# Kernel tuning notes

Hardware: AMD Instinct MI355X
Metric: run time of the kernel (lower is better)

Reference implementation:

```python
import jax, jax.numpy as jnp
import numpy as np

H = 512; W = 512; C = 32; E = 32; NH = 2; HD = 16; B = 4; N = 50000
SHIFTS = jnp.array([[0, 0], [-1, 0], [1, 0], [0, 1], [-1, 1], [1, 1], [0, -1], [-1, -1], [1, -1]], dtype=jnp.int32)


def setup_inputs() -> dict:
    key = jax.random.key(0)
    ks = jax.random.split(key, 12)

    def coords(k):
        # unique BEV cells per sample -> well-defined coord->index lookup
        flat = jax.random.permutation(k, H * W)[:N]
        return jnp.stack([flat // W, flat % W], axis=-1).astype(jnp.int32)

    li_coors = jnp.stack([coords(jax.random.fold_in(ks[0], b)) for b in range(B)])
    ra_coors = jnp.stack([coords(jax.random.fold_in(ks[1], b)) for b in range(B)])
    li_feats = jax.random.normal(ks[2], (B, N, C), jnp.float32)
    ra_feats = jax.random.normal(ks[3], (B, N, C), jnp.float32)
    s = 0.1
    return {
        "li_feats": li_feats, "li_coors": li_coors,
        "ra_feats": ra_feats, "ra_coors": ra_coors,
        "w_qkv1": jax.random.normal(ks[4], (3 * E, E), jnp.float32) * s,
        "b_qkv1": jax.random.normal(ks[5], (3 * E,), jnp.float32) * s,
        "w_out1": jax.random.normal(ks[6], (E, E), jnp.float32) * s,
        "b_out1": jax.random.normal(ks[7], (E,), jnp.float32) * s,
        "w_qkv2": jax.random.normal(ks[8], (3 * E, E), jnp.float32) * s,
        "b_qkv2": jax.random.normal(ks[9], (3 * E,), jnp.float32) * s,
        "w_out2": jax.random.normal(ks[10], (E, E), jnp.float32) * s,
        "b_out2": jax.random.normal(ks[11], (E,), jnp.float32) * s,
    }


def _mha(q, kv, w_qkv, b_qkv, w_out, b_out):
    # q: [N,1,E], kv: [N,9,E]; torch MultiheadAttention (eval, dropout off)
    wq, wk, wv = jnp.split(w_qkv, 3, axis=0)
    bq, bk, bv = jnp.split(b_qkv, 3)
    n = q.shape[0]
    Q = (q @ wq.T + bq).reshape(n, 1, NH, HD)
    K = (kv @ wk.T + bk).reshape(n, 9, NH, HD)
    V = (kv @ wv.T + bv).reshape(n, 9, NH, HD)
    s = jnp.einsum('nqhd,nkhd->nhqk', Q, K) / jnp.sqrt(jnp.float32(HD))
    a = jax.nn.softmax(s, axis=-1)
    o = jnp.einsum('nhqk,nkhd->nqhd', a, V).reshape(n, E)
    return o @ w_out.T + b_out


def _gather_keys(q_coor, kv_coor, kv_feat):
    # dense grid lookup: BEV cell -> voxel index in kv (-1 if empty)
    nk = kv_coor.shape[0]
    grid = jnp.full((H * W,), -1, jnp.int32).at[kv_coor[:, 0] * W + kv_coor[:, 1]].set(
        jnp.arange(nk, dtype=jnp.int32))
    sh = q_coor[:, None, :] + SHIFTS[None]  # [N,9,2]
    valid = (sh[..., 0] >= 0) & (sh[..., 0] < H) & (sh[..., 1] >= 0) & (sh[..., 1] < W)
    flat = jnp.clip(sh[..., 0], 0, H - 1) * W + jnp.clip(sh[..., 1], 0, W - 1)
    idx = jnp.where(valid, grid[flat], -1)  # [N,9]
    keys = jnp.where((idx >= 0)[..., None], kv_feat[jnp.clip(idx, 0)], 0.0)
    return keys  # [N,9,C]


def _scatter(feat, coor):
    # PointPillarsScatter: place [N,C] voxel feats into dense [C,H,W] canvas
    flat = coor[:, 0] * W + coor[:, 1]
    return jnp.zeros((C, H * W), feat.dtype).at[:, flat].set(feat.T).reshape(C, H, W)


def _branch(q_feat, q_coor, kv_feat, kv_coor, w_qkv, b_qkv, w_out, b_out):
    keys = _gather_keys(q_coor, kv_coor, kv_feat)
    out = _mha(q_feat[:, None, :], keys, w_qkv, b_qkv, w_out, b_out)
    return _scatter(q_feat + out, q_coor)


def reference(li_feats, li_coors, ra_feats, ra_coors,
              w_qkv1, b_qkv1, w_out1, b_out1,
              w_qkv2, b_qkv2, w_out2, b_out2):
    vb = jax.vmap(_branch, in_axes=(0, 0, 0, 0, None, None, None, None))
    li_img = vb(li_feats, li_coors, ra_feats, ra_coors, w_qkv1, b_qkv1, w_out1, b_out1)
    ra_img = vb(ra_feats, ra_coors, li_feats, li_coors, w_qkv2, b_qkv2, w_out2, b_out2)
    return (li_img, ra_img)  # each [B, C, H, W]
```

## Files before the change

### kernel.cpp

```cpp
#include <hip/hip_runtime.h>

#define HH 512
#define WW 512
#define HWC (HH * WW)
#define NV 50000
#define NB 4
#define NR (NB * NV)
#define NQ (2 * NR)
#define KVROWS (NR + 1)

typedef unsigned int uint32;

static __device__ __forceinline__ float4 ld4(const float* p) {
    return *reinterpret_cast<const float4*>(p);
}
static __device__ __forceinline__ uint32 bf16rne(float x) {
    uint32 u = __float_as_uint(x);
    return (u + 0x7FFFu + ((u >> 16) & 1u)) >> 16;
}

static __device__ __forceinline__ float red16(float x) {
    float t;
    t = __int_as_float(__builtin_amdgcn_update_dpp(0, __float_as_int(x), 0xB1, 0xF, 0xF, true));
    x += t;
    t = __int_as_float(__builtin_amdgcn_update_dpp(0, __float_as_int(x), 0x4E, 0xF, 0xF, true));
    x += t;
    t = __int_as_float(__builtin_amdgcn_update_dpp(0, __float_as_int(x), 0x141, 0xF, 0xF, true));
    x += t;
    t = __int_as_float(__builtin_amdgcn_update_dpp(0, __float_as_int(x), 0x140, 0xF, 0xF, true));
    x += t;
    return x;
}

__global__ void k_fill(int4* __restrict__ p) {
    const int total = 2 * NB * HWC / 4;
    const int stride = gridDim.x * blockDim.x;
    const int4 v = make_int4(-1, -1, -1, -1);
    for (int i = blockIdx.x * blockDim.x + threadIdx.x; i < total; i += stride)
        p[i] = v;
}

__global__ void k_grid(const int* __restrict__ li_coors, const int* __restrict__ ra_coors,
                       int* __restrict__ grids) {
    int t = blockIdx.x * blockDim.x + threadIdx.x;
    if (t >= NQ) return;
    int set = t / NR;
    int r2 = t - set * NR;
    int b = r2 / NV;
    int n = r2 - b * NV;
    const int* co = (set == 0 ? li_coors : ra_coors) + (size_t)(b * NV + n) * 2;
    grids[(set * NB + b) * HWC + co[0] * WW + co[1]] = n;
}

__launch_bounds__(256)
__global__ void k_proj_kv(const float* __restrict__ li_feats, const float* __restrict__ ra_feats,
                          const float* __restrict__ w_qkv1, const float* __restrict__ b_qkv1,
                          const float* __restrict__ w_qkv2, const float* __restrict__ b_qkv2,
                          uint32* __restrict__ KV) {
    const int f = blockIdx.y;
    const float* feats = f ? ra_feats : li_feats;
    const float* wkv_g = f ? w_qkv1 : w_qkv2;
    const float* bkv_g = f ? b_qkv1 : b_qkv2;

    __shared__ float xs[4][2][64];
    const int wave = threadIdx.x >> 6;
    const int l    = threadIdx.x & 63;
    const int h    = l >> 5;
    const int j    = l & 31;

    const int gw = blockIdx.x * 4 + wave;
    const int gs = gridDim.x * 4;

    int r0 = gw * 2;
    float xreg = feats[(size_t)r0 * 32 + l];

    float4 wk[8], wv[8];
#pragma unroll
    for (int i = 0; i < 8; ++i) {
        wk[i] = ld4(wkv_g + (32 + j) * 32 + i * 4);
        wv[i] = ld4(wkv_g + (64 + j) * 32 + i * 4);
    }
    const float bk = bkv_g[32 + j], bv = bkv_g[64 + j];

    uint32* KVb = KV + (size_t)(f ^ 1) * KVROWS * 32;

    if (blockIdx.x == 0 && threadIdx.x < 32)
        KVb[(size_t)NR * 32 + threadIdx.x] = bf16rne(bk) | (bf16rne(bv) << 16);

    int cur = 0;
    while (r0 < NR) {
        xs[wave][cur][l] = xreg;
        const int rn = r0 + gs * 2;
        if (rn < NR) xreg = feats[(size_t)rn * 32 + l];

        const float* xp = &xs[wave][cur][h * 32];
        float ak = bk, av = bv;
#pragma unroll
        for (int i = 0; i < 8; ++i) {
            float4 x = *reinterpret_cast<const float4*>(xp + i * 4);
            ak += x.x * wk[i].x + x.y * wk[i].y + x.z * wk[i].z + x.w * wk[i].w;
            av += x.x * wv[i].x + x.y * wv[i].y + x.z * wv[i].z + x.w * wv[i].w;
        }
        KVb[(size_t)(r0 + h) * 32 + j] = bf16rne(ak) | (bf16rne(av) << 16);
        r0 = rn;
        cur ^= 1;
    }
}

__global__ void k_nbr(const int* __restrict__ li_coors, const int* __restrict__ ra_coors,
                      const int* __restrict__ grids, int* __restrict__ nbr) {
    int q = blockIdx.x * 256 + threadIdx.x;
    if (q >= NQ) return;
    int br  = (q >= NR) ? 1 : 0;
    int rem = q - br * NR;
    int b   = rem / NV;
    const int* qc = br ? ra_coors : li_coors;
    const int* kvgrid = grids + ((br ^ 1) * NB + b) * HWC;
    const int2 rc = *reinterpret_cast<const int2*>(qc + (size_t)rem * 2);

    const int drs[9] = {0, -1, 1, 0, -1, 1, 0, -1, 1};
    const int dcs[9] = {0, 0, 0, 1, 1, 1, -1, -1, -1};
    const int base = b * NV;
    int v[9];
#pragma unroll
    for (int k = 0; k < 9; ++k) {
        int rr = rc.x + drs[k], cc = rc.y + dcs[k];
        bool valid = ((unsigned)rr < HH) & ((unsigned)cc < WW);
        int raw = kvgrid[valid ? rr * WW + cc : 0];
        int id = valid ? raw : -1;
        v[k] = (id >= 0 ? base + id : NR) * 128;
    }
    int4* np = reinterpret_cast<int4*>(nbr + (size_t)q * 12);
    np[0] = make_int4(v[0], v[1], v[2], v[3]);
    np[1] = make_int4(v[4], v[5], v[6], v[7]);
    np[2] = make_int4(v[8], 0, 0, 0);
}

__launch_bounds__(256)
__global__ void k_attn(const int* __restrict__ nbr,
                       const float* __restrict__ li_feats, const float* __restrict__ ra_feats,
                       const float* __restrict__ w_qkv1, const float* __restrict__ b_qkv1,
                       const float* __restrict__ w_out1, const float* __restrict__ b_out1,
                       const float* __restrict__ w_qkv2, const float* __restrict__ b_qkv2,
                       const float* __restrict__ w_out2, const float* __restrict__ b_out2,
                       const uint32* __restrict__ KV, float* __restrict__ res) {
    __shared__ float xs[8][4][32];
    __shared__ float os[8][4][32];
    const int g = threadIdx.x >> 5;
    const int j = threadIdx.x & 31;
    const int q0 = (blockIdx.x * 8 + g) * 4;
    const int br  = (q0 >= NR) ? 1 : 0;
    const int rem = q0 - br * NR;
    const float* feats = br ? ra_feats : li_feats;
    const float* wqkv  = br ? w_qkv2 : w_qkv1;
    const float* bqkv  = br ? b_qkv2 : b_qkv1;
    const float* wout  = br ? w_out2 : w_out1;
    const float* bout  = br ? b_out2 : b_out1;
    const char* KVbr = (const char*)(KV + (size_t)br * KVROWS * 32);

    int4 a0[4], a1[4], a2[4];
#pragma unroll
    for (int u = 0; u < 4; ++u) {
        const int4* np = reinterpret_cast<const int4*>(nbr + (size_t)(q0 + u) * 12);
        a0[u] = np[0]; a1[u] = np[1]; a2[u] = np[2];
    }

    float fr[4];
#pragma unroll
    for (int u = 0; u < 4; ++u) {
        fr[u] = feats[(size_t)(rem + u) * 32 + j];
        xs[g][u][j] = fr[u];
    }

    const int joff = j * 4;
    uint32 kvw[4][9];
#pragma unroll
    for (int u = 0; u < 4; ++u) {
        int off[9] = {a0[u].x, a0[u].y, a0[u].z, a0[u].w,
                      a1[u].x, a1[u].y, a1[u].z, a1[u].w, a2[u].x};
#pragma unroll
        for (int k = 0; k < 9; ++k)
            kvw[u][k] = *reinterpret_cast<const uint32*>(KVbr + (size_t)(unsigned)(off[k] + joff));
    }

    const float bq = bqkv[j];
    float Qf[4] = {bq, bq, bq, bq};
#pragma unroll
    for (int i = 0; i < 8; ++i) {
        float4 w = ld4(wqkv + j * 32 + i * 4);
#pragma unroll
        for (int u = 0; u < 4; ++u) {
            float4 x = *reinterpret_cast<const float4*>(&xs[g][u][i * 4]);
            Qf[u] += x.x * w.x + x.y * w.y + x.z * w.z + x.w * w.w;
        }
    }
    const float SC = 0.25f * 1.44269504f;
#pragma unroll
    for (int u = 0; u < 4; ++u) Qf[u] *= SC;

#pragma unroll
    for (int u = 0; u < 4; ++u) {
        float sum = 0.f, o = 0.f;
#pragma unroll
        for (int k = 0; k < 9; ++k) {
            float kk = __uint_as_float(kvw[u][k] << 16);
            float e = exp2f(red16(Qf[u] * kk));
            float vv = __uint_as_float(kvw[u][k] & 0xFFFF0000u);
            sum += e;
            o += e * vv;
        }
        os[g][u][j] = o / sum;
    }

    const float bo = bout[j];
    float outv[4] = {bo, bo, bo, bo};
#pragma unroll
    for (int i = 0; i < 8; ++i) {
        float4 w = ld4(wout + j * 32 + i * 4);
#pragma unroll
        for (int u = 0; u < 4; ++u) {
            float4 x = *reinterpret_cast<const float4*>(&os[g][u][i * 4]);
            outv[u] += x.x * w.x + x.y * w.y + x.z * w.z + x.w * w.w;
        }
    }
#pragma unroll
    for (int u = 0; u < 4; ++u)
        res[(size_t)(q0 + u) * 32 + j] = fr[u] + outv[u];
}

__launch_bounds__(256)
__global__ void k_densify(const int* __restrict__ grids, const float* __restrict__ res,
                          float* __restrict__ out) {
    int t = blockIdx.x * 256 + threadIdx.x;
    int plane = t >> 18;
    int s = t & (HWC - 1);
    int gidx = grids[t];
    float4 v[8];
    if (gidx >= 0) {
        const float* rp = res + ((size_t)plane * NV + gidx) * 32;
#pragma unroll
        for (int i = 0; i < 8; ++i) v[i] = ld4(rp + i * 4);
    } else {
#pragma unroll
        for (int i = 0; i < 8; ++i) v[i] = make_float4(0.f, 0.f, 0.f, 0.f);
    }
    float* ob = out + (size_t)plane * 32 * HWC + s;
#pragma unroll
    for (int i = 0; i < 8; ++i) {
        __builtin_nontemporal_store(v[i].x, ob + (size_t)(4 * i + 0) * HWC);
        __builtin_nontemporal_store(v[i].y, ob + (size_t)(4 * i + 1) * HWC);
        __builtin_nontemporal_store(v[i].z, ob + (size_t)(4 * i + 2) * HWC);
        __builtin_nontemporal_store(v[i].w, ob + (size_t)(4 * i + 3) * HWC);
    }
}

extern "C" void kernel_launch(void* const* d_in, const int* in_sizes, int n_in,
                              void* d_out, int out_size, void* d_ws, size_t ws_size,
                              hipStream_t stream) {
    const float* li_feats = (const float*)d_in[0];
    const int*   li_coors = (const int*)d_in[1];
    const float* ra_feats = (const float*)d_in[2];
    const int*   ra_coors = (const int*)d_in[3];
    const float* w_qkv1 = (const float*)d_in[4];
    const float* b_qkv1 = (const float*)d_in[5];
    const float* w_out1 = (const float*)d_in[6];
    const float* b_out1 = (const float*)d_in[7];
    const float* w_qkv2 = (const float*)d_in[8];
    const float* b_qkv2 = (const float*)d_in[9];
    const float* w_out2 = (const float*)d_in[10];
    const float* b_out2 = (const float*)d_in[11];
    float* out = (float*)d_out;

    char* ws = (char*)d_ws;
    size_t off = 0;
    int*    grids = (int*)(ws + off);    off += (size_t)2 * NB * HWC * 4;
    uint32* KV    = (uint32*)(ws + off); off += (size_t)2 * KVROWS * 32 * 4;
    float*  res   = (float*)(ws + off);  off += (size_t)NQ * 32 * 4;
    int*    nbr   = (int*)(ws + off);    off += (size_t)NQ * 12 * 4;

    k_fill<<<2048, 256, 0, stream>>>((int4*)grids);

    k_grid<<<(NQ + 255) / 256, 256, 0, stream>>>(li_coors, ra_coors, grids);

    k_proj_kv<<<dim3(3200, 2), 256, 0, stream>>>(
        li_feats, ra_feats, w_qkv1, b_qkv1, w_qkv2, b_qkv2, KV);

    k_nbr<<<(NQ + 255) / 256, 256, 0, stream>>>(li_coors, ra_coors, grids, nbr);

    k_attn<<<NQ / 32, 256, 0, stream>>>(
        nbr, li_feats, ra_feats,
        w_qkv1, b_qkv1, w_out1, b_out1,
        w_qkv2, b_qkv2, w_out2, b_out2,
        KV, res);

    k_densify<<<(2 * NB * HWC) / 256, 256, 0, stream>>>(grids, res, out);
}
```

Measured before the change: 272.2 us.

## Remap attention lanes so each handles 4 channels of one query with 16B KV loads

```diff
diff --git a/kernel.cpp b/kernel.cpp
--- a/kernel.cpp
+++ b/kernel.cpp
@@ -18,18 +18,10 @@
     uint32 u = __float_as_uint(x);
     return (u + 0x7FFFu + ((u >> 16) & 1u)) >> 16;
 }
-
-static __device__ __forceinline__ float red16(float x) {
-    float t;
-    t = __int_as_float(__builtin_amdgcn_update_dpp(0, __float_as_int(x), 0xB1, 0xF, 0xF, true));
-    x += t;
-    t = __int_as_float(__builtin_amdgcn_update_dpp(0, __float_as_int(x), 0x4E, 0xF, 0xF, true));
-    x += t;
-    t = __int_as_float(__builtin_amdgcn_update_dpp(0, __float_as_int(x), 0x141, 0xF, 0xF, true));
-    x += t;
-    t = __int_as_float(__builtin_amdgcn_update_dpp(0, __float_as_int(x), 0x140, 0xF, 0xF, true));
-    x += t;
-    return x;
+template <int CTRL>
+static __device__ __forceinline__ float dpp_add(float x) {
+    float t = __int_as_float(__builtin_amdgcn_update_dpp(0, __float_as_int(x), CTRL, 0xF, 0xF, true));
+    return x + t;
 }
 
 __global__ void k_fill(int4* __restrict__ p) {
@@ -145,12 +137,15 @@
                        const float* __restrict__ w_out2, const float* __restrict__ b_out2,
                        const uint32* __restrict__ KV, float* __restrict__ res) {
     __shared__ float xs[8][4][32];
-    __shared__ float os[8][4][32];
-    const int g = threadIdx.x >> 5;
-    const int j = threadIdx.x & 31;
-    const int q0 = (blockIdx.x * 8 + g) * 4;
-    const int br  = (q0 >= NR) ? 1 : 0;
-    const int rem = q0 - br * NR;
+    __shared__ float Qls[4][8][36];
+    __shared__ float os[4][8][36];
+    const int tid = threadIdx.x;
+    const int w = tid >> 6;
+    const int l = tid & 63;
+    const int g = tid >> 5;
+    const int j = tid & 31;
+    const int wq0 = (blockIdx.x * 4 + w) * 8;
+    const int br  = (wq0 >= NR) ? 1 : 0;
     const float* feats = br ? ra_feats : li_feats;
     const float* wqkv  = br ? w_qkv2 : w_qkv1;
     const float* bqkv  = br ? b_qkv2 : b_qkv1;
@@ -158,74 +153,76 @@
     const float* bout  = br ? b_out2 : b_out1;
     const char* KVbr = (const char*)(KV + (size_t)br * KVROWS * 32);
 
-    int4 a0[4], a1[4], a2[4];
+    const int qB = wq0 + (l >> 3);
+    const int4* np = reinterpret_cast<const int4*>(nbr + (size_t)qB * 12);
+    int4 b0 = np[0], b1 = np[1], b2 = np[2];
+    const int coff = (l & 7) * 16;
+    int off[9] = {b0.x, b0.y, b0.z, b0.w, b1.x, b1.y, b1.z, b1.w, b2.x};
+    uint4 kv4[9];
+#pragma unroll
+    for (int k = 0; k < 9; ++k)
+        kv4[k] = *reinterpret_cast<const uint4*>(KVbr + (size_t)(unsigned)(off[k] + coff));
+
+    const int qrow = (l >> 5) << 2;
+    const int remA = wq0 + qrow - br * NR;
+    float fr[4];
 #pragma unroll
     for (int u = 0; u < 4; ++u) {
-        const int4* np = reinterpret_cast<const int4*>(nbr + (size_t)(q0 + u) * 12);
-        a0[u] = np[0]; a1[u] = np[1]; a2[u] = np[2];
-    }
-
-    float fr[4];
-#pragma unroll
-    for (int u = 0; u < 4; ++u) {
-        fr[u] = feats[(size_t)(rem + u) * 32 + j];
+        fr[u] = feats[(size_t)(remA + u) * 32 + j];
         xs[g][u][j] = fr[u];
     }
-
-    const int joff = j * 4;
-    uint32 kvw[4][9];
-#pragma unroll
-    for (int u = 0; u < 4; ++u) {
-        int off[9] = {a0[u].x, a0[u].y, a0[u].z, a0[u].w,
-                      a1[u].x, a1[u].y, a1[u].z, a1[u].w, a2[u].x};
-#pragma unroll
-        for (int k = 0; k < 9; ++k)
-            kvw[u][k] = *reinterpret_cast<const uint32*>(KVbr + (size_t)(unsigned)(off[k] + joff));
-    }
-
     const float bq = bqkv[j];
     float Qf[4] = {bq, bq, bq, bq};
 #pragma unroll
     for (int i = 0; i < 8; ++i) {
-        float4 w = ld4(wqkv + j * 32 + i * 4);
+        float4 wv4 = ld4(wqkv + j * 32 + i * 4);
 #pragma unroll
         for (int u = 0; u < 4; ++u) {
             float4 x = *reinterpret_cast<const float4*>(&xs[g][u][i * 4]);
-            Qf[u] += x.x * w.x + x.y * w.y + x.z * w.z + x.w * w.w;
+            Qf[u] += x.x * wv4.x + x.y * wv4.y + x.z * wv4.z + x.w * wv4.w;
         }
     }
     const float SC = 0.25f * 1.44269504f;
 #pragma unroll
-    for (int u = 0; u < 4; ++u) Qf[u] *= SC;
-
-#pragma unroll
-    for (int u = 0; u < 4; ++u) {
-        float sum = 0.f, o = 0.f;
-#pragma unroll
-        for (int k = 0; k < 9; ++k) {
-            float kk = __uint_as_float(kvw[u][k] << 16);
-            float e = exp2f(red16(Qf[u] * kk));
-            float vv = __uint_as_float(kvw[u][k] & 0xFFFF0000u);
-            sum += e;
-            o += e * vv;
-        }
-        os[g][u][j] = o / sum;
-    }
+    for (int u = 0; u < 4; ++u) Qls[w][qrow + u][j] = Qf[u] * SC;
+
+    float4 q4 = *reinterpret_cast<const float4*>(&Qls[w][l >> 3][(l & 7) * 4]);
+    float o0 = 0.f, o1 = 0.f, o2 = 0.f, o3 = 0.f, sum = 0.f;
+#pragma unroll
+    for (int k = 0; k < 9; ++k) {
+        uint4 c = kv4[k];
+        float k0 = __uint_as_float(c.x << 16);
+        float k1 = __uint_as_float(c.y << 16);
+        float k2 = __uint_as_float(c.z << 16);
+        float k3 = __uint_as_float(c.w << 16);
+        float d = q4.x * k0 + q4.y * k1 + q4.z * k2 + q4.w * k3;
+        d = dpp_add<0xB1>(d);
+        d = dpp_add<0x4E>(d);
+        float e = exp2f(d);
+        sum += e;
+        o0 += e * __uint_as_float(c.x & 0xFFFF0000u);
+        o1 += e * __uint_as_float(c.y & 0xFFFF0000u);
+        o2 += e * __uint_as_float(c.z & 0xFFFF0000u);
+        o3 += e * __uint_as_float(c.w & 0xFFFF0000u);
+    }
+    const float rs = 1.0f / sum;
+    *reinterpret_cast<float4*>(&os[w][l >> 3][(l & 7) * 4]) =
+        make_float4(o0 * rs, o1 * rs, o2 * rs, o3 * rs);
 
     const float bo = bout[j];
     float outv[4] = {bo, bo, bo, bo};
 #pragma unroll
     for (int i = 0; i < 8; ++i) {
-        float4 w = ld4(wout + j * 32 + i * 4);
+        float4 wv4 = ld4(wout + j * 32 + i * 4);
 #pragma unroll
         for (int u = 0; u < 4; ++u) {
-            float4 x = *reinterpret_cast<const float4*>(&os[g][u][i * 4]);
-            outv[u] += x.x * w.x + x.y * w.y + x.z * w.z + x.w * w.w;
+            float4 x = *reinterpret_cast<const float4*>(&os[w][qrow + u][i * 4]);
+            outv[u] += x.x * wv4.x + x.y * wv4.y + x.z * wv4.z + x.w * wv4.w;
         }
     }
 #pragma unroll
     for (int u = 0; u < 4; ++u)
-        res[(size_t)(q0 + u) * 32 + j] = fr[u] + outv[u];
+        res[(size_t)(wq0 + qrow + u) * 32 + j] = fr[u] + outv[u];
 }
 
 __launch_bounds__(256)
```

After: 258.0 us. 1.05x faster.
